# Performance work log

Hardware: AMD Instinct MI355X
Metric: run time of the kernel (lower is better)

Reference implementation:

```python
import jax, jax.numpy as jnp
import numpy as np

DG = 8      # deformable groups
K = 3       # deform kernel size
K2 = K * K
CPG = 64 // DG  # input channels per deformable group


def conv2d(x, w, b, pad):
    out = jax.lax.conv_general_dilated(
        x, w, window_strides=(1, 1), padding=[(pad, pad), (pad, pad)],
        dimension_numbers=('NCHW', 'OIHW', 'NCHW'))
    return out + b[None, :, None, None]


def resize_axis(x, out_len, axis):
    # PyTorch bilinear, align_corners=False (half-pixel centers, src clamped >= 0)
    in_len = x.shape[axis]
    src = (jnp.arange(out_len, dtype=jnp.float32) + 0.5) * (in_len / out_len) - 0.5
    src = jnp.maximum(src, 0.0)
    i0 = jnp.floor(src).astype(jnp.int32)
    i1 = jnp.minimum(i0 + 1, in_len - 1)
    t = src - i0.astype(jnp.float32)
    a = jnp.take(x, i0, axis=axis)
    c = jnp.take(x, i1, axis=axis)
    shp = [1] * x.ndim
    shp[axis] = out_len
    t = t.reshape(shp)
    return a * (1.0 - t) + c * t


def bilinear_resize(x, H, W):
    return resize_axis(resize_axis(x, H, 2), W, 3)


def modulated_deform_conv(y, off, msk, w, b):
    # y: [B,C,H,W]; off: [B,DG*2*K2,H,W] (per kernel pt: dy then dx);
    # msk: [B,DG*K2,H,W]; w: [O,C,K,K]; stride=1, pad=K//2, dilation=1.
    B, C, H, W = y.shape
    off = off.reshape(B, DG, K2, 2, H, W)
    off_y, off_x = off[:, :, :, 0], off[:, :, :, 1]      # [B,DG,K2,H,W]
    msk = msk.reshape(B, DG, K2, H, W)

    ky, kx = jnp.meshgrid(jnp.arange(K), jnp.arange(K), indexing='ij')
    kdy = (ky.reshape(-1) - K // 2).astype(jnp.float32)  # kernel y displacement
    kdx = (kx.reshape(-1) - K // 2).astype(jnp.float32)
    hh = jnp.arange(H, dtype=jnp.float32)[:, None]
    ww = jnp.arange(W, dtype=jnp.float32)[None, :]
    py = hh[None, None, None] + kdy[None, None, :, None, None] + off_y  # [B,DG,K2,H,W]
    px = ww[None, None, None] + kdx[None, None, :, None, None] + off_x

    y0 = jnp.floor(py)
    x0 = jnp.floor(px)
    ty = py - y0
    tx = px - x0
    y0i = y0.astype(jnp.int32)
    x0i = x0.astype(jnp.int32)

    yg = y.reshape(B, DG, CPG, H * W)

    def gather(yi, xi):
        valid = ((yi >= 0) & (yi < H) & (xi >= 0) & (xi < W)).astype(y.dtype)
        idx = jnp.clip(yi, 0, H - 1) * W + jnp.clip(xi, 0, W - 1)  # [B,DG,K2,H,W]
        idxf = jnp.broadcast_to(idx.reshape(B, DG, 1, K2 * H * W),
                                (B, DG, CPG, K2 * H * W))
        v = jnp.take_along_axis(yg, idxf, axis=3).reshape(B, DG, CPG, K2, H, W)
        return v * valid[:, :, None]

    v00 = gather(y0i, x0i)
    v01 = gather(y0i, x0i + 1)
    v10 = gather(y0i + 1, x0i)
    v11 = gather(y0i + 1, x0i + 1)

    wy = ty[:, :, None]  # [B,DG,1,K2,H,W]
    wx = tx[:, :, None]
    val = (v00 * (1 - wy) * (1 - wx) + v01 * (1 - wy) * wx
           + v10 * wy * (1 - wx) + v11 * wy * wx)
    val = val * msk[:, :, None]

    wk = w.reshape(w.shape[0], DG, CPG, K2)  # [O,DG,CPG,K2]
    out = jnp.einsum('bgckhw,ogck->bohw', val, wk) + b[None, :, None, None]
    return out


def setup_inputs() -> dict:
    key = jax.random.key(0)
    ks = jax.random.split(key, 6)
    in_nc, out_nc, deform_nc = 64, 64, 64
    om_ch = DG * 3 * K2  # 216
    x = jax.random.normal(ks[0], (4, in_nc, 48, 48), dtype=jnp.float32)
    y = jax.random.normal(ks[1], (4, deform_nc, 96, 96), dtype=jnp.float32)
    w_om = jax.random.normal(ks[2], (om_ch, in_nc, 3, 3), dtype=jnp.float32) * 0.04
    b_om = jax.random.normal(ks[3], (om_ch,), dtype=jnp.float32) * 0.04
    w_dc = jax.random.normal(ks[4], (out_nc, deform_nc, K, K), dtype=jnp.float32) * 0.04
    b_dc = jax.random.normal(ks[5], (out_nc,), dtype=jnp.float32) * 0.04
    return {"x": x, "y": y, "w_om": w_om, "b_om": b_om, "w_dc": w_dc, "b_dc": b_dc}


def reference(x, y, w_om, b_om, w_dc, b_dc):
    B, _, Hy, Wy = y.shape
    off_msk = conv2d(x, w_om, b_om, pad=1)                 # [B,DG*3*K2,Hx,Wx]
    off_msk = bilinear_resize(off_msk, Hy, Wy)             # to y's spatial size
    off = off_msk[:, :DG * 2 * K2]
    msk = jax.nn.sigmoid(off_msk[:, DG * 2 * K2:])
    return jax.nn.relu(modulated_deform_conv(y, off, msk, w_dc, b_dc))
```

## Files before the change

kernel.cpp:

```cpp
#include <hip/hip_runtime.h>
#include <math.h>

#define HX 48
#define WX 48
#define OMC 216
#define HY 96
#define WY 96

typedef __attribute__((ext_vector_type(8))) short bf16x8;
typedef __attribute__((ext_vector_type(4))) float f32x4;

__device__ inline unsigned short f2bf(float f) {
  unsigned u = __float_as_uint(f);
  return (unsigned short)((u + 0x7fffu + ((u >> 16) & 1u)) >> 16);
}
__device__ inline unsigned pk2(float a, float b) {
  return (unsigned)f2bf(a) | ((unsigned)f2bf(b) << 16);
}


__global__ __launch_bounds__(256) void prep_ytr_kernel(
    const float* __restrict__ w_om, const float* __restrict__ w_dc,
    const float* __restrict__ y,
    unsigned short* __restrict__ ap2, unsigned short* __restrict__ ap1,
    float* __restrict__ yt) {
  __shared__ float tile[64][65];
  int bid = blockIdx.x;
  int t = threadIdx.x;
  if (bid < 720) {
    int idx = bid * 256 + t;
    if (idx < 147456) {
      int j = idx & 7;
      int tmp = idx >> 3;
      int l = tmp & 63; tmp >>= 6;
      int m = tmp & 15; tmp >>= 4;
      int s = tmp % 6, p = tmp / 6;
      int oc = m * 16 + (l & 15);
      int kk = s * 32 + (l >> 4) * 8 + j;
      int tap = kk >> 6, c = kk & 63;
      int k = p * 3 + tap;
      ap2[idx] = (oc < OMC) ? f2bf(w_om[oc * 576 + c * 9 + k]) : (unsigned short)0;
    } else {
      int i2 = idx - 147456;
      int j = i2 & 7;
      int tmp = i2 >> 3;
      int l = tmp & 63; tmp >>= 6;
      int w = tmp & 3; tmp >>= 2;
      int s = tmp % 6, p = tmp / 6;
      int oc = w * 16 + (l & 15);
      int kk = s * 32 + (l >> 4) * 8 + j;
      int tap = kk >> 6, c = kk & 63;
      ap1[i2] = f2bf(w_dc[oc * 576 + c * 9 + p * 3 + tap]);
    }
  } else {
    int blk = bid - 720;
    int b = blk / 144;
    int p0 = (blk % 144) * 64;
    int pl = t & 63;
    int cb = t >> 6;
#pragma unroll
    for (int i = 0; i < 16; ++i) {
      int c = cb * 16 + i;
      tile[c][pl] = y[((size_t)(b * 64 + c)) * 9216 + p0 + pl];
    }
    __syncthreads();
    int cw = t & 63;
    int pb = t >> 6;
#pragma unroll
    for (int i = 0; i < 16; ++i) {
      int p = pb * 16 + i;
      yt[((size_t)(b * 9216 + p0 + p)) * 64 + cw] = tile[cw][p];
    }
  }
}

__global__ __launch_bounds__(256) void conv_mfma_kernel(
    const float* __restrict__ x, const unsigned short* __restrict__ ap2,
    const float* __restrict__ bom, float* __restrict__ om) {
  __shared__ unsigned short sB[9][16][72];
  int t = threadIdx.x;
  int bid = blockIdx.x;
  int logical = (bid & 7) * 144 + (bid >> 3);
  int och = logical / 576;
  int rem = logical % 576;
  int b = rem / 144;
  int tl = rem % 144;
  int h0 = (tl / 12) * 4;
  int w0 = (tl % 12) * 4;
  int s_ic = t >> 2;
  int s_row = t & 3;
  const float* xp = x + (size_t)b * 64 * 2304 + (size_t)s_ic * 2304;

  float4 X[3][3];
  bool hvr[3];
#pragma unroll
  for (int r = 0; r < 3; ++r) {
    int hh = h0 + s_row + r - 1;
    hvr[r] = (unsigned)hh < (unsigned)HX;
    int hc = min(max(hh, 0), HX - 1);
    const float* xr = xp + hc * WX;
#pragma unroll
    for (int q = 0; q < 3; ++q) {
      int cb = min(max(w0 - 4 + 4 * q, 0), WX - 4);
      X[r][q] = *(const float4*)&xr[cb];
    }
  }
#pragma unroll
  for (int k = 0; k < 9; ++k) {
    int dy = k / 3 - 1, dx = k % 3 - 1;
    int r = dy + 1;
#pragma unroll
    for (int j = 0; j < 4; ++j) {
      int idx = j + dx + 4;
      int q = idx >> 2, e = idx & 3;
      float val = (e == 0) ? X[r][q].x : (e == 1) ? X[r][q].y
                : (e == 2) ? X[r][q].z : X[r][q].w;
      bool cv = (unsigned)(w0 + j + dx) < (unsigned)WX;
      float v = (hvr[r] && cv) ? val : 0.f;
      sB[k][s_row * 4 + j][s_ic] = f2bf(v);
    }
  }
  __syncthreads();

  int w = t >> 6;
  int l = t & 63;
  int lr = l & 15;
  int lg = l >> 4;
  f32x4 acc[2] = {};
#pragma unroll
  for (int p = 0; p < 3; ++p) {
#pragma unroll
    for (int s = 0; s < 6; ++s) {
      int tapidx = p * 3 + (s >> 1);
      int c0 = (s & 1) * 32;
      bf16x8 bv = *(const bf16x8*)&sB[tapidx][lr][c0 + lg * 8];
#pragma unroll
      for (int m = 0; m < 2; ++m) {
        int mq = och * 8 + w * 2 + m;
        bf16x8 av = *(const bf16x8*)(ap2 +
            (size_t)((((p * 6 + s) * 16) + mq) * 64 + l) * 8);
        acc[m] = __builtin_amdgcn_mfma_f32_16x16x32_bf16(av, bv, acc[m], 0, 0, 0);
      }
    }
  }
  int prow = lr >> 2, pcol = lr & 3;
#pragma unroll
  for (int m = 0; m < 2; ++m) {
    int ocb = (och * 8 + w * 2 + m) * 16 + lg * 4;
    if (ocb < OMC) {
      float4 bb = *(const float4*)&bom[ocb];
      float bvv[4] = {bb.x, bb.y, bb.z, bb.w};
#pragma unroll
      for (int i = 0; i < 4; ++i) {
        om[((size_t)(b * OMC + ocb + i)) * 2304 + (h0 + prow) * WX + w0 + pcol] =
            acc[m][i] + bvv[i];
      }
    }
  }
}

#define MAD4(d, s, mw)                                                  \
  d.x += (mw) * s.x; d.y += (mw) * s.y; d.z += (mw) * s.z; d.w += (mw) * s.w;

__global__ __launch_bounds__(256) void deform_mfma_kernel(
    const float* __restrict__ yt, const float* __restrict__ om,
    const unsigned short* __restrict__ ap1, const float* __restrict__ bdc,
    float* __restrict__ out) {
  __shared__ float sTy[72][16];
  __shared__ float sTx[72][16];
  __shared__ float sTm[72][16];
  __shared__ unsigned short sval[2][16][72];
  int t = threadIdx.x;
  int bid = blockIdx.x;
  int logical = (bid & 7) * 288 + (bid >> 3);
  int b = logical / 576;
  int tl = logical % 576;
  int h0 = (tl / 24) * 4;
  int w0 = (tl % 24) * 4;
  const float* omb = om + (size_t)b * OMC * 2304;
  const float* ytb = yt + (size_t)b * 9216 * 64;

#pragma unroll
  for (int r = 0; r < 5; ++r) {
    int j = t + r * 256;
    if (j < 1152) {
      int k = j >> 7;
      int g = (j >> 4) & 7;
      int px = j & 15;
      int gh = h0 + (px >> 2);
      int gw = w0 + (px & 3);
      float sh = fmaxf(gh * 0.5f - 0.25f, 0.f);
      float sw = fmaxf(gw * 0.5f - 0.25f, 0.f);
      int i0h = (int)sh; float th = sh - (float)i0h;
      int i0w = (int)sw; float tw = sw - (float)i0w;
      int i1h = min(i0h + 1, HX - 1);
      int i1w = min(i0w + 1, WX - 1);
      float r00 = (1.f - th) * (1.f - tw), r01 = (1.f - th) * tw;
      float r10 = th * (1.f - tw),         r11 = th * tw;
      int a00 = i0h * WX + i0w, a01 = i0h * WX + i1w;
      int a10 = i1h * WX + i0w, a11 = i1h * WX + i1w;
      const float* cy = omb + (size_t)(g * 18 + k * 2) * 2304;
      const float* cx = cy + 2304;
      const float* cm = omb + (size_t)(144 + g * 9 + k) * 2304;
      float oy = r00 * cy[a00] + r01 * cy[a01] + r10 * cy[a10] + r11 * cy[a11];
      float ox = r00 * cx[a00] + r01 * cx[a01] + r10 * cx[a10] + r11 * cx[a11];
      float mv = r00 * cm[a00] + r01 * cm[a01] + r10 * cm[a10] + r11 * cm[a11];
      int row = k * 8 + g;
      sTy[row][px] = (float)(gh + k / 3 - 1) + oy;
      sTx[row][px] = (float)(gw + k % 3 - 1) + ox;
      sTm[row][px] = 1.f / (1.f + __expf(-mv));
    }
  }

  int item = t >> 1;
  int g = item >> 4;
  int px = item & 15;
  int cp = t & 1;
  int chb = g * 8 + cp * 4;

  int w = t >> 6;
  int l = t & 63;
  int lr = l & 15;
  int lg = l >> 4;

  __syncthreads();

  float4 C[2][4];
  float W[2][4];

  auto issueC = [&](int k, float4* Co, float* Wo) {
    int row = k * 8 + g;
    float py = sTy[row][px], pxf = sTx[row][px], m = sTm[row][px];
    float y0f = floorf(py), x0f = floorf(pxf);
    float ty = py - y0f, tx = pxf - x0f;
    int y0 = (int)y0f, x0 = (int)x0f;
    int y1 = y0 + 1, x1 = x0 + 1;
    float w00 = (1.f - ty) * (1.f - tx) * m, w01 = (1.f - ty) * tx * m;
    float w10 = ty * (1.f - tx) * m,         w11 = ty * tx * m;
    Wo[0] = ((unsigned)y0 < HY && (unsigned)x0 < WY) ? w00 : 0.f;
    Wo[1] = ((unsigned)y0 < HY && (unsigned)x1 < WY) ? w01 : 0.f;
    Wo[2] = ((unsigned)y1 < HY && (unsigned)x0 < WY) ? w10 : 0.f;
    Wo[3] = ((unsigned)y1 < HY && (unsigned)x1 < WY) ? w11 : 0.f;
    int y0c = min(max(y0, 0), HY - 1), y1c = min(max(y1, 0), HY - 1);
    int x0c = min(max(x0, 0), WY - 1), x1c = min(max(x1, 0), WY - 1);
    Co[0] = *(const float4*)(ytb + (size_t)(y0c * WY + x0c) * 64 + chb);
    Co[1] = *(const float4*)(ytb + (size_t)(y0c * WY + x1c) * 64 + chb);
    Co[2] = *(const float4*)(ytb + (size_t)(y1c * WY + x0c) * 64 + chb);
    Co[3] = *(const float4*)(ytb + (size_t)(y1c * WY + x1c) * 64 + chb);
  };
  auto finishC = [&](const float4* Ci, const float* Wi, int buf) {
    float4 s0 = {0, 0, 0, 0};
    MAD4(s0, Ci[0], Wi[0]) MAD4(s0, Ci[1], Wi[1])
    MAD4(s0, Ci[2], Wi[2]) MAD4(s0, Ci[3], Wi[3])
    *(uint2*)&sval[buf][px][chb] = make_uint2(pk2(s0.x, s0.y), pk2(s0.z, s0.w));
  };

  issueC(0, C[0], W[0]);
  __builtin_amdgcn_sched_barrier(0);

  f32x4 acc = {};
#pragma unroll
  for (int tp = 0; tp < 9; ++tp) {
    if (tp + 1 < 9) {
      issueC(tp + 1, C[(tp + 1) & 1], W[(tp + 1) & 1]);
      __builtin_amdgcn_sched_barrier(0);
    }
    finishC(C[tp & 1], W[tp & 1], tp & 1);
    __syncthreads();
    int p = tp / 3;
    int sl = (tp % 3) * 2;
#pragma unroll
    for (int half = 0; half < 2; ++half) {
      int s = sl + half;
      bf16x8 av = *(const bf16x8*)(ap1 +
          (size_t)(((p * 6 + s) * 4 + w) * 64 + l) * 8);
      bf16x8 bv = *(const bf16x8*)&sval[tp & 1][lr][half * 32 + lg * 8];
      acc = __builtin_amdgcn_mfma_f32_16x16x32_bf16(av, bv, acc, 0, 0, 0);
    }
  }

  float4 bb = *(const float4*)&bdc[w * 16 + lg * 4];
  float bvv[4] = {bb.x, bb.y, bb.z, bb.w};
#pragma unroll
  for (int i = 0; i < 4; ++i) {
    int oc = w * 16 + lg * 4 + i;
    out[((size_t)(b * 64 + oc) * 96 + h0 + (lr >> 2)) * 96 + w0 + (lr & 3)] =
        fmaxf(acc[i] + bvv[i], 0.f);
  }
}

extern "C" void kernel_launch(void* const* d_in, const int* in_sizes, int n_in,
                              void* d_out, int out_size, void* d_ws, size_t ws_size,
                              hipStream_t stream) {
  const float* x = (const float*)d_in[0];
  const float* y = (const float*)d_in[1];
  const float* w_om = (const float*)d_in[2];
  const float* b_om = (const float*)d_in[3];
  const float* w_dc = (const float*)d_in[4];
  const float* b_dc = (const float*)d_in[5];
  float* out = (float*)d_out;

  float* om  = (float*)d_ws;
  unsigned short* ap2 = (unsigned short*)(om + 1990656);
  unsigned short* ap1 = ap2 + 147456;
  float* yt  = (float*)(ap1 + 36864);

  prep_ytr_kernel<<<1296, 256, 0, stream>>>(w_om, w_dc, y, ap2, ap1, yt);
  conv_mfma_kernel<<<1152, 256, 0, stream>>>(x, ap2, b_om, om);
  deform_mfma_kernel<<<2304, 256, 0, stream>>>(yt, om, ap1, b_dc, out);
}
```

Baseline: 64.89 us.

## Store transposed y in bf16 and stage a 12x12 halo window in LDS

The transpose kernel now writes the channels-last copy of y as bf16 instead of fp32, which halves its write traffic and the deform kernel's gather traffic. The deform kernel preloads a 12x12-pixel, 64-channel bf16 window around its 4x4 tile into XOR-swizzled shared memory. Each bilinear corner is read from LDS when it falls inside that window and from global memory otherwise. The explicit double-buffered prefetch of corner loads is dropped, and rounding y to bf16 before interpolation adds precision loss.

```diff
diff --git a/kernel.cpp b/kernel.cpp
--- a/kernel.cpp
+++ b/kernel.cpp
@@ -23,7 +23,7 @@
     const float* __restrict__ w_om, const float* __restrict__ w_dc,
     const float* __restrict__ y,
     unsigned short* __restrict__ ap2, unsigned short* __restrict__ ap1,
-    float* __restrict__ yt) {
+    unsigned short* __restrict__ ytbf) {
   __shared__ float tile[64][65];
   int bid = blockIdx.x;
   int t = threadIdx.x;
@@ -69,7 +69,7 @@
 #pragma unroll
     for (int i = 0; i < 16; ++i) {
       int p = pb * 16 + i;
-      yt[((size_t)(b * 9216 + p0 + p)) * 64 + cw] = tile[cw][p];
+      ytbf[((size_t)(b * 9216 + p0 + p)) * 64 + cw] = f2bf(tile[cw][p]);
     }
   }
 }
@@ -159,13 +159,11 @@
   }
 }
 
-#define MAD4(d, s, mw)                                                  \
-  d.x += (mw) * s.x; d.y += (mw) * s.y; d.z += (mw) * s.z; d.w += (mw) * s.w;
-
 __global__ __launch_bounds__(256) void deform_mfma_kernel(
-    const float* __restrict__ yt, const float* __restrict__ om,
+    const unsigned short* __restrict__ ytbf, const float* __restrict__ om,
     const unsigned short* __restrict__ ap1, const float* __restrict__ bdc,
     float* __restrict__ out) {
+  __shared__ unsigned short sYt[144 * 64];
   __shared__ float sTy[72][16];
   __shared__ float sTx[72][16];
   __shared__ float sTm[72][16];
@@ -177,8 +175,19 @@
   int tl = logical % 576;
   int h0 = (tl / 24) * 4;
   int w0 = (tl % 24) * 4;
+  int wy0 = min(max(h0 - 4, 0), HY - 12);
+  int wx0 = min(max(w0 - 4, 0), WY - 12);
   const float* omb = om + (size_t)b * OMC * 2304;
-  const float* ytb = yt + (size_t)b * 9216 * 64;
+  const unsigned short* ytb = ytbf + (size_t)b * 9216 * 64;
+
+  for (int i = t; i < 1152; i += 256) {
+    int pxl = i >> 3, part = i & 7;
+    int ry = pxl / 12, rx = pxl - ry * 12;
+    const unsigned short* src =
+        ytb + ((size_t)((wy0 + ry) * WY + wx0 + rx) << 6) + part * 8;
+    int gr = part ^ (pxl & 7);
+    *(uint4*)&sYt[pxl * 64 + gr * 8] = *(const uint4*)src;
+  }
 
 #pragma unroll
   for (int r = 0; r < 5; ++r) {
@@ -225,11 +234,10 @@
 
   __syncthreads();
 
-  float4 C[2][4];
-  float W[2][4];
-
-  auto issueC = [&](int k, float4* Co, float* Wo) {
-    int row = k * 8 + g;
+  f32x4 acc = {};
+#pragma unroll
+  for (int tp = 0; tp < 9; ++tp) {
+    int row = tp * 8 + g;
     float py = sTy[row][px], pxf = sTx[row][px], m = sTm[row][px];
     float y0f = floorf(py), x0f = floorf(pxf);
     float ty = py - y0f, tx = pxf - x0f;
@@ -237,35 +245,33 @@
     int y1 = y0 + 1, x1 = x0 + 1;
     float w00 = (1.f - ty) * (1.f - tx) * m, w01 = (1.f - ty) * tx * m;
     float w10 = ty * (1.f - tx) * m,         w11 = ty * tx * m;
-    Wo[0] = ((unsigned)y0 < HY && (unsigned)x0 < WY) ? w00 : 0.f;
-    Wo[1] = ((unsigned)y0 < HY && (unsigned)x1 < WY) ? w01 : 0.f;
-    Wo[2] = ((unsigned)y1 < HY && (unsigned)x0 < WY) ? w10 : 0.f;
-    Wo[3] = ((unsigned)y1 < HY && (unsigned)x1 < WY) ? w11 : 0.f;
-    int y0c = min(max(y0, 0), HY - 1), y1c = min(max(y1, 0), HY - 1);
-    int x0c = min(max(x0, 0), WY - 1), x1c = min(max(x1, 0), WY - 1);
-    Co[0] = *(const float4*)(ytb + (size_t)(y0c * WY + x0c) * 64 + chb);
-    Co[1] = *(const float4*)(ytb + (size_t)(y0c * WY + x1c) * 64 + chb);
-    Co[2] = *(const float4*)(ytb + (size_t)(y1c * WY + x0c) * 64 + chb);
-    Co[3] = *(const float4*)(ytb + (size_t)(y1c * WY + x1c) * 64 + chb);
-  };
-  auto finishC = [&](const float4* Ci, const float* Wi, int buf) {
-    float4 s0 = {0, 0, 0, 0};
-    MAD4(s0, Ci[0], Wi[0]) MAD4(s0, Ci[1], Wi[1])
-    MAD4(s0, Ci[2], Wi[2]) MAD4(s0, Ci[3], Wi[3])
-    *(uint2*)&sval[buf][px][chb] = make_uint2(pk2(s0.x, s0.y), pk2(s0.z, s0.w));
-  };
-
-  issueC(0, C[0], W[0]);
-  __builtin_amdgcn_sched_barrier(0);
-
-  f32x4 acc = {};
-#pragma unroll
-  for (int tp = 0; tp < 9; ++tp) {
-    if (tp + 1 < 9) {
-      issueC(tp + 1, C[(tp + 1) & 1], W[(tp + 1) & 1]);
-      __builtin_amdgcn_sched_barrier(0);
-    }
-    finishC(C[tp & 1], W[tp & 1], tp & 1);
+    float W0 = ((unsigned)y0 < HY && (unsigned)x0 < WY) ? w00 : 0.f;
+    float W1 = ((unsigned)y0 < HY && (unsigned)x1 < WY) ? w01 : 0.f;
+    float W2 = ((unsigned)y1 < HY && (unsigned)x0 < WY) ? w10 : 0.f;
+    float W3 = ((unsigned)y1 < HY && (unsigned)x1 < WY) ? w11 : 0.f;
+    float4 s0 = {0.f, 0.f, 0.f, 0.f};
+
+    auto corner = [&](int yy, int xx, float wgt) {
+      int ly = yy - wy0, lx = xx - wx0;
+      ushort4 v;
+      if ((unsigned)ly < 12u && (unsigned)lx < 12u) {
+        int pxl = ly * 12 + lx;
+        v = *(const ushort4*)&sYt[pxl * 64 + ((g ^ (pxl & 7)) << 3) + cp * 4];
+      } else {
+        int yc = min(max(yy, 0), HY - 1), xc = min(max(xx, 0), WY - 1);
+        v = *(const ushort4*)&ytb[((size_t)(yc * WY + xc) << 6) + chb];
+      }
+      s0.x += wgt * __uint_as_float((unsigned)v.x << 16);
+      s0.y += wgt * __uint_as_float((unsigned)v.y << 16);
+      s0.z += wgt * __uint_as_float((unsigned)v.z << 16);
+      s0.w += wgt * __uint_as_float((unsigned)v.w << 16);
+    };
+    corner(y0, x0, W0);
+    corner(y0, x1, W1);
+    corner(y1, x0, W2);
+    corner(y1, x1, W3);
+
+    *(uint2*)&sval[tp & 1][px][chb] = make_uint2(pk2(s0.x, s0.y), pk2(s0.z, s0.w));
     __syncthreads();
     int p = tp / 3;
     int sl = (tp % 3) * 2;
@@ -303,9 +309,9 @@
   float* om  = (float*)d_ws;
   unsigned short* ap2 = (unsigned short*)(om + 1990656);
   unsigned short* ap1 = ap2 + 147456;
-  float* yt  = (float*)(ap1 + 36864);
-
-  prep_ytr_kernel<<<1296, 256, 0, stream>>>(w_om, w_dc, y, ap2, ap1, yt);
+  unsigned short* ytbf = ap1 + 36864;
+
+  prep_ytr_kernel<<<1296, 256, 0, stream>>>(w_om, w_dc, y, ap2, ap1, ytbf);
   conv_mfma_kernel<<<1152, 256, 0, stream>>>(x, ap2, b_om, om);
-  deform_mfma_kernel<<<2304, 256, 0, stream>>>(yt, om, ap1, b_dc, out);
-}
+  deform_mfma_kernel<<<2304, 256, 0, stream>>>(ytbf, om, ap1, b_dc, out);
+}
```

Result: faster. 63.12 us (-2.7%).
